# Performance work log

Hardware: AMD Instinct MI355X
Metric: run time of the kernel (lower is better)

The kernel has to match this reference:

```python
import jax, jax.numpy as jnp
from jax import lax
import numpy as np

B, S, H, L = 128, 256, 768, 24


def setup_inputs() -> dict:
    key = jax.random.key(0)
    k_tf, k_len, k_w, k_tr, k_st, k_en = jax.random.split(key, 6)
    token_features = jax.random.normal(k_tf, (B, S, H), dtype=jnp.float32)
    # contiguous valid lengths in [3, S] (>=3 so that stripping CLS/SEP leaves >=1 token)
    lengths = jax.random.randint(k_len, (B,), 3, S + 1)
    pos = jnp.arange(S)
    input_mask = (pos[None, :] < lengths[:, None]).astype(jnp.int32)
    true_label_mask = (pos[None, :] < (lengths - 2)[:, None]).astype(jnp.int32)
    W = jax.random.normal(k_w, (H, L), dtype=jnp.float32) * 0.02
    b = jnp.zeros((L,), dtype=jnp.float32)
    transitions = jax.random.normal(k_tr, (L, L), dtype=jnp.float32) * 0.1
    start_trans = jax.random.normal(k_st, (L,), dtype=jnp.float32) * 0.1
    end_trans = jax.random.normal(k_en, (L,), dtype=jnp.float32) * 0.1
    return {
        "token_features": token_features,
        "input_mask": input_mask,
        "true_label_mask": true_label_mask,
        "W": W,
        "b": b,
        "transitions": transitions,
        "start_trans": start_trans,
        "end_trans": end_trans,
    }


def _compact(x, mask):
    """Vectorized version of the torch per-token copy loop: for each row,
    gather valid tokens (mask==1) preserving order, drop the first and last
    valid token (CLS/SEP), left-pack into a zero tensor."""
    # stable argsort puts valid positions first, in order
    order = jnp.argsort(1 - mask.astype(jnp.int32), axis=1)  # [B,S]
    gathered = jnp.take_along_axis(x, order[:, :, None], axis=1)  # [B,S,H]
    # drop first valid token (shift left by 1), pad a zero row at the end
    shifted = jnp.concatenate([gathered[:, 1:], jnp.zeros_like(gathered[:, :1])], axis=1)
    n_valid = mask.sum(axis=1)  # [B]
    keep = jnp.arange(x.shape[1])[None, :] < (n_valid[:, None] - 2)  # also drops last (SEP)
    return jnp.where(keep[:, :, None], shifted, 0.0)


def _viterbi(emissions, mask, transitions, start_trans, end_trans):
    """Masked Viterbi decode. emissions [B,S,L], mask [B,S] bool."""
    Bn, Sn, Ln = emissions.shape
    lbl = jnp.arange(Ln)
    score0 = start_trans[None, :] + emissions[:, 0]  # [B,L]

    def step(score, xs):
        em_t, m_t = xs  # [B,L], [B]
        cand = score[:, :, None] + transitions[None]  # [B,prev,curr]
        best = cand.max(axis=1) + em_t
        bp = cand.argmax(axis=1)  # [B,L] best prev tag per curr tag
        new_score = jnp.where(m_t[:, None], best, score)
        bp = jnp.where(m_t[:, None], bp, lbl[None, :])  # identity backpointer on pad
        return new_score, bp

    ems = jnp.swapaxes(emissions[:, 1:], 0, 1)  # [S-1,B,L]
    ms = jnp.swapaxes(mask[:, 1:], 0, 1)  # [S-1,B]
    final, bps = lax.scan(step, score0, (ems, ms))
    final = final + end_trans[None, :]
    best_score = final.max(axis=1)  # [B]
    last_tag = final.argmax(axis=1)  # [B]

    def back(tag, bp):  # tag: tag at time t; bp: bp_t -> tag at t-1
        prev = jnp.take_along_axis(bp, tag[:, None], axis=1)[:, 0]
        return prev, tag

    tag0, tags_rest = lax.scan(back, last_tag, bps, reverse=True)  # tags_rest [S-1,B]
    path = jnp.concatenate([tag0[:, None], jnp.swapaxes(tags_rest, 0, 1)], axis=1)  # [B,S]
    return best_score, path


def reference(token_features, input_mask, true_label_mask, W, b, transitions, start_trans, end_trans):
    mask = input_mask.astype(bool)
    wv = _compact(token_features, mask)  # dropout is identity at inference
    emissions = jax.nn.sigmoid(wv @ W + b)  # [B,S,L]
    _, path = _viterbi(emissions, true_label_mask != 0, transitions, start_trans, end_trans)
    return path
```

## Files before the change

### kernel.cpp

```cpp
#include <hip/hip_runtime.h>
#include <math.h>

#define NB 128
#define NS 256
#define NH 768
#define NL 24
#define ASTR 68

__global__ __launch_bounds__(256) void ner_emis(
    const float* __restrict__ tf, const int* __restrict__ tlm,
    const float* __restrict__ W, const float* __restrict__ bias,
    float* __restrict__ E)
{
    const int b    = blockIdx.x >> 3;
    const int tile = (blockIdx.x & 7) << 5;
    const int tid  = threadIdx.x;
    if (tlm[b*NS + tile] == 0) return;

    __shared__ float lds[8*32*25];
    float* As = lds;
    float* Ws = lds + 32*ASTR;
    float* Pr = lds;

    const int tok  = tid & 15;
    const int ksub = tid >> 4;
    const int kk   = ksub << 2;
    const int rot  = ksub & 3;

    float acc0[NL], acc1[NL];
    #pragma unroll
    for (int l = 0; l < NL; ++l) { acc0[l] = 0.f; acc1[l] = 0.f; }

    const float* tfb = tf + (size_t)(b*NS)*NH;

    const int rowA0 = tid >> 4,            c4A0 = tid & 15;
    const int rowA1 = (tid + 256) >> 4,    c4A1 = tid & 15;
    int trow0 = tile + rowA0 + 1; if (trow0 > 255) trow0 = 255;
    int trow1 = tile + rowA1 + 1; if (trow1 > 255) trow1 = 255;
    const float* srcA0 = tfb + (size_t)trow0*NH + (c4A0 << 2);
    const float* srcA1 = tfb + (size_t)trow1*NH + (c4A1 << 2);

    float4 pa0, pa1, pw0, pw1;
    pa0 = *(const float4*)(srcA0);
    pa1 = *(const float4*)(srcA1);
    {
        const float4* wsrc = (const float4*)(W);
        pw0 = wsrc[tid];
        if (tid < 128) pw1 = wsrc[tid + 256];
    }
    {
        float* d0 = As + rowA0*ASTR + (c4A0 << 2);
        d0[0]=pa0.x; d0[1]=pa0.y; d0[2]=pa0.z; d0[3]=pa0.w;
        float* d1 = As + rowA1*ASTR + (c4A1 << 2);
        d1[0]=pa1.x; d1[1]=pa1.y; d1[2]=pa1.z; d1[3]=pa1.w;
        ((float4*)Ws)[tid] = pw0;
        if (tid < 128) ((float4*)Ws)[tid + 256] = pw1;
    }
    __syncthreads();

    for (int kc0 = 0; kc0 < NH; kc0 += 64) {
        const bool more = (kc0 + 64 < NH);
        if (more) {
            pa0 = *(const float4*)(srcA0 + kc0 + 64);
            pa1 = *(const float4*)(srcA1 + kc0 + 64);
            const float4* wsrc = (const float4*)(W + (size_t)(kc0 + 64)*NL);
            pw0 = wsrc[tid];
            if (tid < 128) pw1 = wsrc[tid + 256];
        }

        const float* A0 = As + tok*ASTR + kk;
        const float* A1 = A0 + 16*ASTR;
        const float* Wr = Ws + kk*NL;
        #pragma unroll
        for (int s = 0; s < 4; ++s) {
            const int j = (s + rot) & 3;
            float a0 = A0[j];
            float a1 = A1[j];
            const float4* w4 = (const float4*)(Wr + j*NL);
            float wv[NL];
            #pragma unroll
            for (int i = 0; i < 6; ++i) {
                float4 w = w4[i];
                wv[4*i+0] = w.x; wv[4*i+1] = w.y; wv[4*i+2] = w.z; wv[4*i+3] = w.w;
            }
            #pragma unroll
            for (int l = 0; l < NL; ++l) {
                acc0[l] = fmaf(a0, wv[l], acc0[l]);
                acc1[l] = fmaf(a1, wv[l], acc1[l]);
            }
        }
        __syncthreads();

        if (more) {
            float* d0 = As + rowA0*ASTR + (c4A0 << 2);
            d0[0]=pa0.x; d0[1]=pa0.y; d0[2]=pa0.z; d0[3]=pa0.w;
            float* d1 = As + rowA1*ASTR + (c4A1 << 2);
            d1[0]=pa1.x; d1[1]=pa1.y; d1[2]=pa1.z; d1[3]=pa1.w;
            ((float4*)Ws)[tid] = pw0;
            if (tid < 128) ((float4*)Ws)[tid + 256] = pw1;
            __syncthreads();
        }
    }

    if (ksub >= 8) {
        float* p = Pr + ((ksub-8)*32 + tok)*25;
        float* q = p + 16*25;
        #pragma unroll
        for (int l = 0; l < NL; ++l) { p[l] = acc0[l]; q[l] = acc1[l]; }
    }
    __syncthreads();
    if (ksub < 8) {
        const float* p = Pr + (ksub*32 + tok)*25;
        const float* q = p + 16*25;
        #pragma unroll
        for (int l = 0; l < NL; ++l) { acc0[l] += p[l]; acc1[l] += q[l]; }
    }
    __syncthreads();
    if (ksub < 8) {
        float* p = Pr + (ksub*32 + tok)*25;
        float* q = p + 16*25;
        #pragma unroll
        for (int l = 0; l < NL; ++l) { p[l] = acc0[l]; q[l] = acc1[l]; }
    }
    __syncthreads();

    const int* tm = tlm + b*NS + tile;
    float* Eb = E + (size_t)(b*NS + tile)*NL;
    #pragma unroll
    for (int i = 0; i < 3; ++i) {
        int o = tid + (i << 8);
        int t = o / NL, l = o % NL;
        if (tm[t]) {
            float s = 0.f;
            #pragma unroll
            for (int ks = 0; ks < 8; ++ks)
                s += Pr[(ks*32 + t)*25 + l];
            float x = s + bias[l];
            Eb[t*NL + l] = 1.0f/(1.0f + expf(-x));
        }
    }
}

__global__ __launch_bounds__(256) void ner_viterbi(
    const float* __restrict__ E, const int* __restrict__ tlm,
    const float* __restrict__ trans, const float* __restrict__ st,
    const float* __restrict__ en, int* __restrict__ out)
{
    const int tid = threadIdx.x;
    const int b   = blockIdx.x;
    const int bS  = b*NS;

    __shared__ float Esh[NS*NL];
    __shared__ float scl[NS*NL];
    __shared__ float Tt[NL*NL];
    __shared__ float fin[NL];
    __shared__ unsigned char tr_s[NL][NS];
    __shared__ int chosen[12];
    __shared__ int nsh, ltag;

    {
        const float4* src = (const float4*)(E + (size_t)bS*NL);
        float4* dst = (float4*)Esh;
        #pragma unroll
        for (int j = 0; j < 6; ++j) dst[tid + (j << 8)] = src[tid + (j << 8)];
    }
    for (int i = tid; i < NL*NL; i += 256) {
        int c = i / NL, p = i % NL;
        Tt[i] = trans[p*NL + c];
    }
    if (tid < 64) {
        int a = tlm[bS+tid] + tlm[bS+tid+64] + tlm[bS+tid+128] + tlm[bS+tid+192];
        #pragma unroll
        for (int off = 32; off > 0; off >>= 1) a += __shfl_down(a, off, 64);
        if (tid == 0) nsh = a;
    }
    __syncthreads();
    const int n = nsh;

    if (tid < 24) {
        const int c = tid;
        float Tc[24];
        #pragma unroll
        for (int p = 0; p < 24; ++p) Tc[p] = trans[p*NL + c];

        auto bp = [](int idx4, float v) {
            return __int_as_float(__builtin_amdgcn_ds_bpermute(idx4, __float_as_int(v)));
        };

        float sv = st[c] + Esh[c];
        scl[c] = sv;

        auto step = [&](int t, float em) {
            float scr[24];
            #pragma unroll
            for (int p = 0; p < 24; ++p) scr[p] = bp(p << 2, sv);
            float cand[24];
            #pragma unroll
            for (int p = 0; p < 24; ++p) cand[p] = scr[p] + Tc[p];
            float m0 = fmaxf(fmaxf(cand[0],  cand[1]),  cand[2]);
            float m1 = fmaxf(fmaxf(cand[3],  cand[4]),  cand[5]);
            float m2 = fmaxf(fmaxf(cand[6],  cand[7]),  cand[8]);
            float m3 = fmaxf(fmaxf(cand[9],  cand[10]), cand[11]);
            float m4 = fmaxf(fmaxf(cand[12], cand[13]), cand[14]);
            float m5 = fmaxf(fmaxf(cand[15], cand[16]), cand[17]);
            float m6 = fmaxf(fmaxf(cand[18], cand[19]), cand[20]);
            float m7 = fmaxf(fmaxf(cand[21], cand[22]), cand[23]);
            float q0 = fmaxf(fmaxf(m0, m1), m2);
            float q1 = fmaxf(fmaxf(m3, m4), m5);
            float q2 = fmaxf(m6, m7);
            float best = fmaxf(fmaxf(q0, q1), q2);
            sv = best + em;
            scl[t*NL + c] = sv;
        };

        int t = 1;
        for (; t + 8 <= n; t += 8) {
            float em[8];
            const float* eb = Esh + t*NL + c;
            #pragma unroll
            for (int j = 0; j < 8; ++j) em[j] = eb[j*NL];
            #pragma unroll
            for (int j = 0; j < 8; ++j) step(t + j, em[j]);
        }
        for (; t < n; ++t) step(t, Esh[t*NL + c]);
        fin[c] = sv + en[c];
    }
    __syncthreads();

    if (tid == 0) {
        float bv = fin[0]; int bt = 0;
        #pragma unroll
        for (int cc = 1; cc < 24; ++cc) { if (fin[cc] > bv) { bv = fin[cc]; bt = cc; } }
        ltag = bt;
    }
    __syncthreads();

    const int K = (n > 1) ? (n - 1 + 9) / 10 : 1;
    if (n > 1 && tid < 240) {
        const int w = tid / 24 + 1, h = tid % 24;
        int tlo = (w-1)*K; if (tlo > n-1) tlo = n-1;
        int thi = w*K;     if (thi > n-1) thi = n-1;
        int cur = h;
        for (int t = thi; t > tlo; --t) {
            const float4* sp = (const float4*)(scl + (t-1)*NL);
            const float4* up = (const float4*)(Tt  + cur*NL);
            float cand[24];
            #pragma unroll
            for (int i = 0; i < 6; ++i) {
                float4 s = sp[i], u = up[i];
                cand[4*i+0] = s.x + u.x;
                cand[4*i+1] = s.y + u.y;
                cand[4*i+2] = s.z + u.z;
                cand[4*i+3] = s.w + u.w;
            }
            float best = cand[0]; int arg = 0;
            #pragma unroll
            for (int p = 1; p < 24; ++p) { if (cand[p] > best) { best = cand[p]; arg = p; } }
            tr_s[h][t-1] = (unsigned char)arg;
            cur = arg;
        }
    }
    __syncthreads();

    if (tid == 0) {
        int cur = ltag;
        for (int w = 10; w >= 1; --w) {
            chosen[w] = cur;
            int tlo = (w-1)*K; if (tlo > n-1) tlo = n-1;
            int thi = w*K;     if (thi > n-1) thi = n-1;
            if (thi > tlo) cur = tr_s[cur][tlo];
        }
    }
    __syncthreads();

    {
        const int t = tid;
        int tag;
        if (t >= n-1) tag = ltag;
        else { int w = t / K + 1; tag = tr_s[chosen[w]][t]; }
        out[bS + t] = tag;
    }
}

extern "C" void kernel_launch(void* const* d_in, const int* in_sizes, int n_in,
                              void* d_out, int out_size, void* d_ws, size_t ws_size,
                              hipStream_t stream) {
    const float* tf    = (const float*)d_in[0];
    const int*   tlm   = (const int*)  d_in[2];
    const float* W     = (const float*)d_in[3];
    const float* bias  = (const float*)d_in[4];
    const float* trans = (const float*)d_in[5];
    const float* st    = (const float*)d_in[6];
    const float* en    = (const float*)d_in[7];
    float* E = (float*)d_ws;

    ner_emis<<<dim3(NB*8), dim3(256), 0, stream>>>(tf, tlm, W, bias, E);
    ner_viterbi<<<dim3(NB), dim3(256), 0, stream>>>(E, tlm, trans, st, en, (int*)d_out);
}
```

Measured before the change: 202.1 us.

## Split Viterbi forward max over two half-waves and combine with permlane32 swap

The forward Viterbi recurrence now uses 64 lanes instead of 24. Each 32-lane half computes the max over 12 of the 24 predecessor labels, so the serial chain of ds_bpermute calls per timestep drops from 24 to 12. The two partial maxima are merged with a cross-half permlane32 swap, with a bpermute fallback when that builtin is missing. The score scratch buffer gets a padded 28-float row stride so the eight extra lanes per half have somewhere to store. In exchange, each step adds a cross-lane exchange and an extra max, and 16 of the lanes do redundant work.

```diff
diff --git a/kernel.cpp b/kernel.cpp
--- a/kernel.cpp
+++ b/kernel.cpp
@@ -6,6 +6,7 @@
 #define NH 768
 #define NL 24
 #define ASTR 68
+#define SCLS 28
 
 __global__ __launch_bounds__(256) void ner_emis(
     const float* __restrict__ tf, const int* __restrict__ tlm,
@@ -151,9 +152,9 @@
     const int bS  = b*NS;
 
     __shared__ float Esh[NS*NL];
-    __shared__ float scl[NS*NL];
+    __shared__ float scl[NS*SCLS];
     __shared__ float Tt[NL*NL];
-    __shared__ float fin[NL];
+    __shared__ float fin[32];
     __shared__ unsigned char tr_s[NL][NS];
     __shared__ int chosen[12];
     __shared__ int nsh, ltag;
@@ -177,53 +178,61 @@
     __syncthreads();
     const int n = nsh;
 
-    if (tid < 24) {
-        const int c = tid;
-        float Tc[24];
-        #pragma unroll
-        for (int p = 0; p < 24; ++p) Tc[p] = trans[p*NL + c];
+    if (tid < 64) {
+        const int lane = tid;
+        const int h    = lane >> 5;
+        const int c    = lane & 31;
+        const int cidx = (c < 24) ? c : 23;
+        const int coff = (c < 24) ? c : 24;
+        const int p0   = h * 12;
+
+        float Tc[12];
+        #pragma unroll
+        for (int j = 0; j < 12; ++j) Tc[j] = trans[(p0 + j)*NL + cidx];
+
+        int idxv[12];
+        #pragma unroll
+        for (int j = 0; j < 12; ++j) idxv[j] = (p0 + j) << 2;
 
         auto bp = [](int idx4, float v) {
             return __int_as_float(__builtin_amdgcn_ds_bpermute(idx4, __float_as_int(v)));
         };
 
-        float sv = st[c] + Esh[c];
-        scl[c] = sv;
+        float sv = st[cidx] + Esh[cidx];
+        scl[coff] = sv;
 
         auto step = [&](int t, float em) {
-            float scr[24];
-            #pragma unroll
-            for (int p = 0; p < 24; ++p) scr[p] = bp(p << 2, sv);
-            float cand[24];
-            #pragma unroll
-            for (int p = 0; p < 24; ++p) cand[p] = scr[p] + Tc[p];
-            float m0 = fmaxf(fmaxf(cand[0],  cand[1]),  cand[2]);
-            float m1 = fmaxf(fmaxf(cand[3],  cand[4]),  cand[5]);
-            float m2 = fmaxf(fmaxf(cand[6],  cand[7]),  cand[8]);
-            float m3 = fmaxf(fmaxf(cand[9],  cand[10]), cand[11]);
-            float m4 = fmaxf(fmaxf(cand[12], cand[13]), cand[14]);
-            float m5 = fmaxf(fmaxf(cand[15], cand[16]), cand[17]);
-            float m6 = fmaxf(fmaxf(cand[18], cand[19]), cand[20]);
-            float m7 = fmaxf(fmaxf(cand[21], cand[22]), cand[23]);
-            float q0 = fmaxf(fmaxf(m0, m1), m2);
-            float q1 = fmaxf(fmaxf(m3, m4), m5);
-            float q2 = fmaxf(m6, m7);
-            float best = fmaxf(fmaxf(q0, q1), q2);
+            float cand[12];
+            #pragma unroll
+            for (int j = 0; j < 12; ++j)
+                cand[j] = bp(idxv[j], sv) + Tc[j];
+            float a0 = fmaxf(fmaxf(cand[0], cand[1]),  cand[2]);
+            float a1 = fmaxf(fmaxf(cand[3], cand[4]),  cand[5]);
+            float a2 = fmaxf(fmaxf(cand[6], cand[7]),  cand[8]);
+            float a3 = fmaxf(fmaxf(cand[9], cand[10]), cand[11]);
+            float pm = fmaxf(fmaxf(a0, a1), fmaxf(a2, a3));
+#if __has_builtin(__builtin_amdgcn_permlane32_swap)
+            auto r = __builtin_amdgcn_permlane32_swap(
+                         __float_as_int(pm), __float_as_int(pm), false, false);
+            float best = fmaxf(__int_as_float(r[0]), __int_as_float(r[1]));
+#else
+            float best = fmaxf(pm, bp((lane ^ 32) << 2, pm));
+#endif
             sv = best + em;
-            scl[t*NL + c] = sv;
+            scl[t*SCLS + coff] = sv;
         };
 
         int t = 1;
         for (; t + 8 <= n; t += 8) {
             float em[8];
-            const float* eb = Esh + t*NL + c;
+            const float* eb = Esh + t*NL + cidx;
             #pragma unroll
             for (int j = 0; j < 8; ++j) em[j] = eb[j*NL];
             #pragma unroll
             for (int j = 0; j < 8; ++j) step(t + j, em[j]);
         }
-        for (; t < n; ++t) step(t, Esh[t*NL + c]);
-        fin[c] = sv + en[c];
+        for (; t < n; ++t) step(t, Esh[t*NL + cidx]);
+        fin[c] = sv + en[cidx];
     }
     __syncthreads();
 
@@ -242,7 +251,7 @@
         int thi = w*K;     if (thi > n-1) thi = n-1;
         int cur = h;
         for (int t = thi; t > tlo; --t) {
-            const float4* sp = (const float4*)(scl + (t-1)*NL);
+            const float4* sp = (const float4*)(scl + (t-1)*SCLS);
             const float4* up = (const float4*)(Tt  + cur*NL);
             float cand[24];
             #pragma unroll
```

Measured after the change: 199.9 us. No clear change (-1.1%).
